# Kernel tuning notes

Hardware: AMD Instinct MI355X
Metric: run time of the kernel (lower is better)

## Reference

```python
import jax, jax.numpy as jnp
import numpy as np

V, E, HD, H, T = 50000, 256, 512, 256, 50  # vocab, embed, hidden_dim, per-direction hidden, tagset
B, S = 128, 512


def setup_inputs() -> dict:
    key = jax.random.key(0)
    ks = jax.random.split(key, 16)
    def n(k, shape, s=0.05):
        return jax.random.normal(k, shape, dtype=jnp.float32) * s
    return {
        "sentences": jax.random.randint(ks[0], (B, S), 0, V),
        "tags": jax.random.randint(ks[1], (B, S), 0, T),
        "mask": jnp.ones((B, S), dtype=bool),
        "embedding": n(ks[2], (V, E), 0.1),
        "w_ih_f": n(ks[3], (4 * H, E)), "w_hh_f": n(ks[4], (4 * H, H)),
        "b_ih_f": n(ks[5], (4 * H,)), "b_hh_f": n(ks[6], (4 * H,)),
        "w_ih_b": n(ks[7], (4 * H, E)), "w_hh_b": n(ks[8], (4 * H, H)),
        "b_ih_b": n(ks[9], (4 * H,)), "b_hh_b": n(ks[10], (4 * H,)),
        "W_out": n(ks[11], (T, HD)), "b_out": n(ks[12], (T,)),
        "start_trans": n(ks[13], (T,), 0.1),
        "end_trans": n(ks[14], (T,), 0.1),
        "trans": n(ks[15], (T, T), 0.1),
    }


def _lstm(xs, w_ih, w_hh, b, reverse):
    # xs: [S, B, E]; PyTorch gate order i, f, g, o
    Hn = w_hh.shape[1]
    def cell(carry, xt):
        h, c = carry
        g = xt @ w_ih.T + h @ w_hh.T + b
        i, f, gg, o = jnp.split(g, 4, axis=-1)
        c = jax.nn.sigmoid(f) * c + jax.nn.sigmoid(i) * jnp.tanh(gg)
        h = jax.nn.sigmoid(o) * jnp.tanh(c)
        return (h, c), h
    z = jnp.zeros((xs.shape[1], Hn), xs.dtype)
    _, hs = jax.lax.scan(cell, (z, z), xs, reverse=reverse)
    return hs  # [S, B, Hn], time-aligned with xs


def reference(sentences, tags, mask, embedding, w_ih_f, w_hh_f, b_ih_f, b_hh_f,
              w_ih_b, w_hh_b, b_ih_b, b_hh_b, W_out, b_out,
              start_trans, end_trans, trans):
    xs = jnp.swapaxes(embedding[sentences], 0, 1)           # [S, B, E]
    hf = _lstm(xs, w_ih_f, w_hh_f, b_ih_f + b_hh_f, False)
    hb = _lstm(xs, w_ih_b, w_hh_b, b_ih_b + b_hh_b, True)
    emis = jnp.concatenate([hf, hb], -1) @ W_out.T + b_out  # [S, B, T]

    tagsT = jnp.swapaxes(tags, 0, 1)                        # [S, B]
    maskT = jnp.swapaxes(mask, 0, 1)                        # [S, B] bool
    mT = maskT.astype(emis.dtype)

    # --- numerator: score of the gold path (first timestep always on, per torchcrf) ---
    emit = jnp.take_along_axis(emis, tagsT[..., None], axis=-1)[..., 0]   # [S, B]
    num = start_trans[tagsT[0]] + emit[0]
    num = num + jnp.sum((trans[tagsT[:-1], tagsT[1:]] + emit[1:]) * mT[1:], axis=0)
    last = jnp.sum(maskT.astype(jnp.int32), axis=0) - 1                    # [B]
    num = num + end_trans[tags[jnp.arange(tags.shape[0]), last]]

    # --- denominator: log-partition via forward algorithm (logsumexp scan) ---
    alpha0 = start_trans[None, :] + emis[0]                 # [B, T]
    def step(alpha, inp):
        e_t, m_t = inp
        nxt = jax.nn.logsumexp(alpha[:, :, None] + trans[None] + e_t[:, None, :], axis=1)
        return jnp.where(m_t[:, None], nxt, alpha), None
    alpha, _ = jax.lax.scan(step, alpha0, (emis[1:], maskT[1:]))
    logZ = jax.nn.logsumexp(alpha + end_trans[None, :], axis=1)

    # model returns -crf(...) with reduction='mean'
    return -jnp.mean(num - logZ)
```

## Files before the change

kernel.cpp:

```cpp
#include <hip/hip_runtime.h>

typedef __bf16 bf16x8 __attribute__((ext_vector_type(8)));
typedef float f32x4 __attribute__((ext_vector_type(4)));
typedef float f32x2 __attribute__((ext_vector_type(2)));
typedef int i32x8 __attribute__((ext_vector_type(8)));
typedef unsigned short ushort_t;
typedef unsigned int u32x4 __attribute__((ext_vector_type(4)));
typedef long i64_t;

constexpr int Ee = 256;
constexpr int HDd = 512;
constexpr int Hh = 256;
constexpr int Tt = 50;
constexpr int Bb = 128;
constexpr int Ss = 512;
constexpr int G4 = 1024;
constexpr int SB = Ss * Bb;
constexpr int Tc = 64;
constexpr int NP = Ss / Tc;
constexpr int HSTR = 272;
constexpr int NSLOT = 16;

constexpr float LOG2E = 1.4426950408889634f;
constexpr float K2f = 2.8853900817779268f;

#define DI __device__ __forceinline__

DI float bf2f(ushort_t u) {
    unsigned int x = ((unsigned int)u) << 16;
    return __builtin_bit_cast(float, x);
}
DI ushort_t f2bf(float f) {
    unsigned int x = __builtin_bit_cast(unsigned int, f);
    x += 0x7fffu + ((x >> 16) & 1u);
    return (ushort_t)(x >> 16);
}
DI bf16x8 cvt8(const float* p) {
    bf16x8 r;
#pragma unroll
    for (int i = 0; i < 8; ++i) r[i] = (__bf16)p[i];
    return r;
}
DI unsigned int pk4_fp8(float a, float b, float c, float d) {
    int v = __builtin_amdgcn_cvt_pk_fp8_f32(a, b, 0, false);
    v = __builtin_amdgcn_cvt_pk_fp8_f32(c, d, v, true);
    return (unsigned int)v;
}
DI unsigned char fp8_1(float a) {
    return (unsigned char)(__builtin_amdgcn_cvt_pk_fp8_f32(a, 0.f, 0, false) & 0xff);
}
DI float rcpf(float x) { return __builtin_amdgcn_rcpf(x); }

#if __has_builtin(__builtin_amdgcn_exp2f)
DI float ex2(float x) { return __builtin_amdgcn_exp2f(x); }
DI float ex2n(float x) { return __builtin_amdgcn_exp2f(-x); }
#else
DI float ex2(float x) {
    float r;
    asm("v_exp_f32 %0, %1\n\ts_nop 0" : "=v"(r) : "v"(x));
    return r;
}
DI float ex2n(float x) {
    float r;
    asm("v_exp_f32 %0, -%1\n\ts_nop 0" : "=v"(r) : "v"(x));
    return r;
}
#endif

DI void lds_barrier() {
    asm volatile("" ::: "memory");
    __builtin_amdgcn_s_waitcnt(0xC07F);
    __builtin_amdgcn_s_barrier();
    asm volatile("" ::: "memory");
}

__global__ void k_prep(const float* __restrict__ wihf, const float* __restrict__ whhf,
                       const float* __restrict__ wihb, const float* __restrict__ whhb,
                       const float* __restrict__ wout,
                       const float* __restrict__ bihf, const float* __restrict__ bhhf,
                       const float* __restrict__ bihb, const float* __restrict__ bhhb,
                       ushort_t* __restrict__ Wihf, ushort_t* __restrict__ Wihb,
                       unsigned char* __restrict__ Whhf8, unsigned char* __restrict__ Whhb8,
                       unsigned char* __restrict__ Wout8,
                       float* __restrict__ biasf, float* __restrict__ biasb,
                       unsigned int* __restrict__ flags) {
    int i = blockIdx.x * 256 + threadIdx.x;
    if (i < G4 * Ee) {
        float s = (((i >> 16) & 3) == 2) ? K2f : LOG2E;
        Wihf[i] = f2bf(wihf[i] * s);
        Wihb[i] = f2bf(wihb[i] * s);
    }
    if (i < G4 * Hh / 4) {
        int base = i * 4;
        float s = (((i >> 14) & 3) == 2) ? K2f : LOG2E;
        ((unsigned int*)Whhf8)[i] = pk4_fp8(whhf[base] * s, whhf[base + 1] * s,
                                            whhf[base + 2] * s, whhf[base + 3] * s);
        ((unsigned int*)Whhb8)[i] = pk4_fp8(whhb[base] * s, whhb[base + 1] * s,
                                            whhb[base + 2] * s, whhb[base + 3] * s);
    }
    if (i < 64 * HDd) Wout8[i] = 0;
    if (i < Tt * HDd) Wout8[i] = fp8_1(wout[i]);
    if (i < G4) {
        float s = (((i >> 8) & 3) == 2) ? K2f : LOG2E;
        biasf[i] = (bihf[i] + bhhf[i]) * s;
        biasb[i] = (bihb[i] + bhhb[i]) * s;
    }
    if (i < 16) flags[i] = 0;
}

struct PhaseArgs {
    const int* sentences;
    const float* emb;
    const ushort_t* Wihf;
    const ushort_t* Wihb;
    const float* biasf;
    const float* biasb;
    const unsigned char* Whhf8;
    const unsigned char* Whhb8;
    unsigned char* Gbuf;
    unsigned char* Hcat8;
    unsigned int* flags;
};

__global__ __launch_bounds__(512, 2) void k_phase(PhaseArgs a) {
    __shared__ unsigned char hring[NSLOT][16][HSTR];
    const size_t CH = (size_t)Tc * Bb * G4;
    int blk = blockIdx.x;
    int tid = threadIdx.x;

    if (blk < 16) {
        int ln = tid & 15, qd = (tid >> 4) & 3, w = tid >> 6;
        int dir = blk >> 3;
        int b0 = (blk & 7) * 16;
        const unsigned char* Whh8 = dir ? a.Whhb8 : a.Whhf8;
        int jc0 = w * 32 + ln;

        i32x8 wreg[2][4][2];
#pragma unroll
        for (int ct = 0; ct < 2; ++ct)
#pragma unroll
            for (int g = 0; g < 4; ++g) {
                const unsigned char* wb = Whh8 + (size_t)(g * Hh + jc0 + ct * 16) * Hh;
#pragma unroll
                for (int ks = 0; ks < 2; ++ks)
                    wreg[ct][g][ks] = *(const i32x8*)(wb + ks * 128 + qd * 32);
            }
        for (int i = tid; i < NSLOT * 16 * HSTR; i += 512) ((unsigned char*)hring)[i] = 0;
        __syncthreads();
        float creg[2][4] = {};
        int sctr = 0;

        for (int p = 0; p < NP; ++p) {
            if (tid == 0) {
                while (__hip_atomic_load(&a.flags[p], __ATOMIC_RELAXED,
                                         __HIP_MEMORY_SCOPE_AGENT) < 240u)
                    __builtin_amdgcn_s_sleep(1);
                __threadfence();
            }
            __syncthreads();

            const unsigned char* G = a.Gbuf + ((size_t)(dir * 2 + (p & 1))) * CH;
            int goff = ((dir ? (Tc - 1) : 0) * 32 + (b0 >> 2) + qd) * 4096 + jc0 * 16;
            const int gstep = dir ? -(32 * 4096) : (32 * 4096);

            u32x4 guA[2], guB[2];
#pragma unroll
            for (int ct = 0; ct < 2; ++ct)
                guA[ct] = *(const u32x4*)(G + goff + ct * 256);

            auto lstm_step = [&](u32x4(&gcur)[2], u32x4(&gnxt)[2], int step) {
                int rslot = (sctr + NSLOT - 1) & (NSLOT - 1), wslot = sctr & (NSLOT - 1);
                int goff2 = goff + gstep;
                if (step + 1 < Tc) {
#pragma unroll
                    for (int ct = 0; ct < 2; ++ct)
                        gnxt[ct] = *(const u32x4*)(G + goff2 + ct * 256);
                }
                i32x8 av2[2];
#pragma unroll
                for (int ks = 0; ks < 2; ++ks)
                    av2[ks] = *(const i32x8*)&hring[rslot][ln][ks * 128 + qd * 32];
                f32x4 acc[2][4];
#pragma unroll
                for (int ct = 0; ct < 2; ++ct)
#pragma unroll
                    for (int g = 0; g < 4; ++g) {
                        f32x2 lo = __builtin_amdgcn_cvt_pk_f32_fp8((int)gcur[ct][g], false);
                        f32x2 hi = __builtin_amdgcn_cvt_pk_f32_fp8((int)gcur[ct][g], true);
                        acc[ct][g][0] = lo[0];
                        acc[ct][g][1] = lo[1];
                        acc[ct][g][2] = hi[0];
                        acc[ct][g][3] = hi[1];
                    }
#pragma unroll
                for (int ks = 0; ks < 2; ++ks)
#pragma unroll
                    for (int ct = 0; ct < 2; ++ct)
#pragma unroll
                        for (int g = 0; g < 4; ++g)
                            acc[ct][g] = __builtin_amdgcn_mfma_scale_f32_16x16x128_f8f6f4(
                                av2[ks], wreg[ct][g][ks], acc[ct][g],
                                0, 0,
                                0, 127,
                                0, 127);
#pragma unroll
                for (int ct = 0; ct < 2; ++ct)
#pragma unroll
                    for (int reg = 0; reg < 4; ++reg) {
                        float ei = ex2n(acc[ct][0][reg]);
                        float ef = ex2n(acc[ct][1][reg]);
                        float eg = ex2(acc[ct][2][reg]);
                        float eo = ex2n(acc[ct][3][reg]);
                        float pf = 1.f + ef;
                        float pig = (1.f + ei) * (eg + 1.f);
                        float t2 = fmaf(eg, K2f, -K2f);
                        float cn = fmaf(creg[ct][reg], pig, t2 * pf) * rcpf(pf * pig);
                        creg[ct][reg] = cn;
                        float ec = ex2(cn);
                        float h = (ec - 1.f) * rcpf((1.f + eo) * (ec + 1.f));
                        hring[wslot][qd * 4 + reg][jc0 + ct * 16] = fp8_1(h);
                    }
                goff = goff2;
                lds_barrier();

                if ((sctr & 7) == 7) {
                    int tbase = sctr - 7;
                    int rid = tid >> 2;
                    int slotidx = rid >> 4, m = rid & 15;
                    int slot = (tbase + slotidx) & (NSLOT - 1);
                    int qp = tid & 3;
                    int t = dir ? (511 - (tbase + slotidx)) : (tbase + slotidx);
                    const unsigned char* src = &hring[slot][m][qp * 64];
                    unsigned char* dst = a.Hcat8 + ((size_t)(t * Bb + b0 + m)) * HDd + dir * Hh + qp * 64;
#pragma unroll
                    for (int i2 = 0; i2 < 4; ++i2) {
                        u32x4 v;
#pragma unroll
                        for (int k = 0; k < 4; ++k)
                            v[k] = *(const unsigned int*)(src + i2 * 16 + k * 4);
                        *(u32x4*)(dst + i2 * 16) = v;
                    }
                }
                ++sctr;
            };

            for (int step = 0; step < Tc; step += 2) {
                lstm_step(guA, guB, step);
                lstm_step(guB, guA, step + 1);
            }

            __syncthreads();
            if (tid == 0) atomicAdd(&a.flags[8 + p], 1u);
        }
    } else {
        int team = tid >> 8;
        int stid = tid & 255;
        int slot = (blk - 16) * 2 + team;
        int ln = stid & 15, qd = (stid >> 4) & 3, wv = stid >> 6;
        for (int q = 0; q < NP; ++q) {
            if (q >= 2) {
                if (tid == 0)
                    while (__hip_atomic_load(&a.flags[8 + q - 2], __ATOMIC_RELAXED,
                                             __HIP_MEMORY_SCOPE_AGENT) < 16u)
                        __builtin_amdgcn_s_sleep(64);
                __syncthreads();
            }
            for (int tile = slot; tile < 1024; tile += 480) {
                int dir = tile >> 9;
                int rem = tile & 511;
                int rt0 = rem >> 3, ct0 = rem & 7;
                const ushort_t* W = dir ? a.Wihb : a.Wihf;
                const float* bias = dir ? a.biasb : a.biasf;
                unsigned char* Gout = a.Gbuf + ((size_t)(dir * 2 + (q & 1))) * CH;
                int t0 = dir ? (NP - 1 - q) * Tc : q * Tc;
                int r0 = rt0 * 128 + (wv & 1) * 64;
                int n0 = ct0 * 128 + (wv >> 1) * 64;
                const float* aptr[4];
#pragma unroll
                for (int rt = 0; rt < 4; ++rt) {
                    int r = r0 + rt * 16 + ln;
                    int t = t0 + (r >> 7), b = r & 127;
                    aptr[rt] = a.emb + (size_t)a.sentences[b * Ss + t] * Ee;
                }
                int wrow[4];
#pragma unroll
                for (int ct = 0; ct < 4; ++ct) {
                    int c = n0 + ct * 16 + ln;
                    wrow[ct] = (c & 3) * 256 + (c >> 2);
                }
                f32x4 acc[4][4] = {};
                for (int ks = 0; ks < 8; ++ks) {
                    int k0 = ks * 32 + qd * 8;
                    bf16x8 av[4], bfr[4];
#pragma unroll
                    for (int rt = 0; rt < 4; ++rt) av[rt] = cvt8(aptr[rt] + k0);
#pragma unroll
                    for (int ct = 0; ct < 4; ++ct)
                        bfr[ct] = *(const bf16x8*)(W + (size_t)wrow[ct] * Ee + k0);
#pragma unroll
                    for (int rt = 0; rt < 4; ++rt)
#pragma unroll
                        for (int ct = 0; ct < 4; ++ct)
                            acc[rt][ct] = __builtin_amdgcn_mfma_f32_16x16x32_bf16(av[rt], bfr[ct], acc[rt][ct], 0, 0, 0);
                }
#pragma unroll
                for (int rt = 0; rt < 4; ++rt)
#pragma unroll
                    for (int ct = 0; ct < 4; ++ct) {
                        int c = n0 + ct * 16 + ln;
                        float bv = bias[wrow[ct]];
                        unsigned int pk = pk4_fp8(acc[rt][ct][0] + bv, acc[rt][ct][1] + bv,
                                                  acc[rt][ct][2] + bv, acc[rt][ct][3] + bv);
                        int rowq = ((r0 + rt * 16) >> 2) + qd;
                        *(unsigned int*)(Gout + (size_t)rowq * 4096 + (size_t)c * 4) = pk;
                    }
            }
            __syncthreads();
            if (tid == 0) {
                __threadfence();
                atomicAdd(&a.flags[q], 1u);
            }
        }
    }
}

__global__ __launch_bounds__(256, 2) void k_emis(const unsigned char* __restrict__ Hcat8,
                                                 const unsigned char* __restrict__ Wout8,
                                                 const float* __restrict__ bout,
                                                 float* __restrict__ emis) {
    int tid = threadIdx.x;
    int ln = tid & 15, qd = (tid >> 4) & 3, w = tid >> 6;
    int r0 = blockIdx.x * 128 + w * 32;
    f32x4 acc[2][4] = {};
    for (int ks = 0; ks < 16; ++ks) {
        int k0 = ks * 32 + qd * 8;
        i64_t av[2], bfr[4];
#pragma unroll
        for (int rt = 0; rt < 2; ++rt)
            av[rt] = *(const i64_t*)(Hcat8 + (size_t)(r0 + rt * 16 + ln) * HDd + k0);
#pragma unroll
        for (int ct = 0; ct < 4; ++ct)
            bfr[ct] = *(const i64_t*)(Wout8 + (size_t)(ct * 16 + ln) * HDd + k0);
#pragma unroll
        for (int rt = 0; rt < 2; ++rt)
#pragma unroll
            for (int ct = 0; ct < 4; ++ct)
                acc[rt][ct] = __builtin_amdgcn_mfma_f32_16x16x32_fp8_fp8(av[rt], bfr[ct], acc[rt][ct], 0, 0, 0);
    }
#pragma unroll
    for (int rt = 0; rt < 2; ++rt)
#pragma unroll
        for (int ct = 0; ct < 4; ++ct) {
            int j = ct * 16 + ln;
            if (j < Tt) {
                float bv = bout[j];
#pragma unroll
                for (int reg = 0; reg < 4; ++reg) {
                    int row = r0 + rt * 16 + qd * 4 + reg;
                    int t = row >> 7, b = row & 127;
                    emis[((size_t)b * Ss + t) * Tt + j] = acc[rt][ct][reg] + bv;
                }
            }
        }
}

__global__ __launch_bounds__(64) void k_crf(const float* __restrict__ emis,
                                            const float* __restrict__ start_trans,
                                            const float* __restrict__ end_trans,
                                            const float* __restrict__ trans,
                                            float* __restrict__ logZ) {
    __shared__ float E_s[64];
    int j = threadIdx.x;
    int b = blockIdx.x;
    const float* eb = emis + (size_t)b * Ss * Tt;

    float preg[52];
    preg[50] = 0.f;
    preg[51] = 0.f;
#pragma unroll
    for (int i = 0; i < Tt; ++i)
        preg[i] = (j < Tt) ? __expf(trans[i * Tt + j]) : 0.f;

    float astart = (j < Tt) ? (start_trans[j] + eb[j]) : 0.f;
    float a0 = __builtin_amdgcn_readfirstlane(astart);
    float vcur = (j < Tt) ? __expf(astart - a0) : 0.f;
    float logacc = a0;
    E_s[j] = vcur;

    float ecur[8], enxt[8];
#pragma unroll
    for (int i = 0; i < 8; ++i)
        ecur[i] = (j < Tt && 1 + i < Ss) ? eb[(1 + i) * Tt + j] : 0.f;

    for (int tb = 1; tb < Ss; tb += 8) {
#pragma unroll
        for (int i = 0; i < 8; ++i) {
            int tn = tb + 8 + i;
            enxt[i] = (j < Tt && tn < Ss) ? eb[(size_t)tn * Tt + j] : 0.f;
        }
        float ex[8];
#pragma unroll
        for (int i = 0; i < 8; ++i) ex[i] = __expf(ecur[i]);
#pragma unroll
        for (int i = 0; i < 8; ++i) {
            int t = tb + i;
            if (t >= Ss) break;
            float s0 = 0.f, s1 = 0.f, s2 = 0.f, s3 = 0.f;
#pragma unroll
            for (int i4 = 0; i4 < 13; ++i4) {
                f32x4 ev = *(const f32x4*)&E_s[i4 * 4];
                s0 = fmaf(ev[0], preg[i4 * 4 + 0], s0);
                s1 = fmaf(ev[1], preg[i4 * 4 + 1], s1);
                s2 = fmaf(ev[2], preg[i4 * 4 + 2], s2);
                s3 = fmaf(ev[3], preg[i4 * 4 + 3], s3);
            }
            vcur = ((s0 + s1) + (s2 + s3)) * ex[i];
            if (i == 3) {
                float n = __builtin_amdgcn_readfirstlane(vcur);
                vcur *= rcpf(n);
                logacc += __logf(n);
            }
            E_s[j] = vcur;
        }
        float n = __builtin_amdgcn_readfirstlane(vcur);
        vcur *= rcpf(n);
        E_s[j] = vcur;
        logacc += __logf(n);
#pragma unroll
        for (int i = 0; i < 8; ++i) ecur[i] = enxt[i];
    }
    float ve = (j < Tt) ? vcur * __expf(end_trans[j]) : 0.f;
    for (int off = 32; off > 0; off >>= 1) ve += __shfl_down(ve, off, 64);
    if (j == 0) logZ[b] = logacc + __logf(ve);
}

__global__ __launch_bounds__(256) void k_num(const int* __restrict__ tags,
                                             const float* __restrict__ emis,
                                             const float* __restrict__ trans,
                                             const float* __restrict__ start_trans,
                                             const float* __restrict__ end_trans,
                                             float* __restrict__ num) {
    __shared__ float red[4];
    int b = blockIdx.x, tid = threadIdx.x;
    const float* eb = emis + (size_t)b * Ss * Tt;
    float v = 0.f;
    for (int t = 1 + tid; t < Ss; t += 256) {
        int tp = tags[b * Ss + t - 1], tc = tags[b * Ss + t];
        v += trans[tp * Tt + tc] + eb[(size_t)t * Tt + tc];
    }
    if (tid == 0) {
        int t0 = tags[b * Ss + 0];
        v += start_trans[t0] + eb[t0] + end_trans[tags[b * Ss + Ss - 1]];
    }
    for (int off = 32; off > 0; off >>= 1) v += __shfl_down(v, off, 64);
    if ((tid & 63) == 0) red[tid >> 6] = v;
    __syncthreads();
    if (tid == 0) num[b] = red[0] + red[1] + red[2] + red[3];
}

__global__ __launch_bounds__(128) void k_out(const float* __restrict__ num,
                                             const float* __restrict__ logZ,
                                             float* __restrict__ out) {
    __shared__ float red[2];
    int b = threadIdx.x;
    float v = num[b] - logZ[b];
    for (int off = 32; off > 0; off >>= 1) v += __shfl_down(v, off, 64);
    if ((b & 63) == 0) red[b >> 6] = v;
    __syncthreads();
    if (b == 0) out[0] = -(red[0] + red[1]) / 128.f;
}

extern "C" void kernel_launch(void* const* d_in, const int* in_sizes, int n_in,
                              void* d_out, int out_size, void* d_ws, size_t ws_size,
                              hipStream_t stream) {
    const int* sentences = (const int*)d_in[0];
    const int* tags = (const int*)d_in[1];
    const float* emb = (const float*)d_in[3];
    const float* wihf = (const float*)d_in[4];
    const float* whhf = (const float*)d_in[5];
    const float* bihf = (const float*)d_in[6];
    const float* bhhf = (const float*)d_in[7];
    const float* wihb = (const float*)d_in[8];
    const float* whhb = (const float*)d_in[9];
    const float* bihb = (const float*)d_in[10];
    const float* bhhb = (const float*)d_in[11];
    const float* wout = (const float*)d_in[12];
    const float* bout = (const float*)d_in[13];
    const float* start_trans = (const float*)d_in[14];
    const float* end_trans = (const float*)d_in[15];
    const float* trans = (const float*)d_in[16];

    char* ws = (char*)d_ws;
    size_t off = 0;
    auto alloc = [&](size_t bytes) {
        void* p = ws + off;
        off += (bytes + 255) & ~(size_t)255;
        return p;
    };
    ushort_t* Wihf = (ushort_t*)alloc((size_t)G4 * Ee * 2);
    ushort_t* Wihb = (ushort_t*)alloc((size_t)G4 * Ee * 2);
    unsigned char* Whhf8 = (unsigned char*)alloc((size_t)G4 * Hh);
    unsigned char* Whhb8 = (unsigned char*)alloc((size_t)G4 * Hh);
    unsigned char* Wout8 = (unsigned char*)alloc((size_t)64 * HDd);
    float* biasf = (float*)alloc(G4 * 4);
    float* biasb = (float*)alloc(G4 * 4);
    unsigned char* Gbuf = (unsigned char*)alloc((size_t)4 * Tc * Bb * G4);
    unsigned char* Hcat8 = (unsigned char*)alloc((size_t)SB * HDd);
    float* emis = (float*)alloc((size_t)SB * Tt * 4);
    float* logZ = (float*)alloc(Bb * 4);
    float* num = (float*)alloc(Bb * 4);
    unsigned int* flags = (unsigned int*)alloc(64 * 4);
    (void)ws_size; (void)in_sizes; (void)n_in; (void)out_size;

    k_prep<<<dim3((G4 * Ee + 255) / 256), dim3(256), 0, stream>>>(
        wihf, whhf, wihb, whhb, wout, bihf, bhhf, bihb, bhhb,
        Wihf, Wihb, Whhf8, Whhb8, Wout8, biasf, biasb, flags);

    PhaseArgs pa;
    pa.sentences = sentences;
    pa.emb = emb;
    pa.Wihf = Wihf;
    pa.Wihb = Wihb;
    pa.biasf = biasf;
    pa.biasb = biasb;
    pa.Whhf8 = Whhf8;
    pa.Whhb8 = Whhb8;
    pa.Gbuf = Gbuf;
    pa.Hcat8 = Hcat8;
    pa.flags = flags;
    void* kargs[] = {&pa};
    hipLaunchCooperativeKernel((void*)k_phase, dim3(256), dim3(512), kargs, 0, stream);

    k_emis<<<dim3(SB / 128), dim3(256), 0, stream>>>(Hcat8, Wout8, bout, emis);

    k_crf<<<dim3(Bb), dim3(64), 0, stream>>>(emis, start_trans, end_trans, trans, logZ);

    k_num<<<dim3(Bb), dim3(256), 0, stream>>>(tags, emis, trans, start_trans, end_trans, num);

    k_out<<<dim3(1), dim3(128), 0, stream>>>(num, logZ, (float*)d_out);
}
```

Measured before the change: 1.301 ms.

## Fuse emission GEMM, CRF forward, numerator and final reduction into persistent cooperative kernel

Moves the emission projection, CRF log-partition scan, gold-path score and final mean into the tail of the cooperative LSTM kernel. Grid-wide atomic flag barriers replace the separate kernel launches. The intent is to remove four launch gaps and the host-side serialization between them. In exchange, the CRF scan now runs on only 64 threads of 128 large blocks, and spin barriers add synchronization cost.

```diff
diff --git a/kernel.cpp b/kernel.cpp
--- a/kernel.cpp
+++ b/kernel.cpp
@@ -105,11 +105,12 @@
         biasf[i] = (bihf[i] + bhhf[i]) * s;
         biasb[i] = (bihb[i] + bhhb[i]) * s;
     }
-    if (i < 16) flags[i] = 0;
+    if (i < 32) flags[i] = 0;
 }
 
 struct PhaseArgs {
     const int* sentences;
+    const int* tags;
     const float* emb;
     const ushort_t* Wihf;
     const ushort_t* Wihb;
@@ -117,8 +118,17 @@
     const float* biasb;
     const unsigned char* Whhf8;
     const unsigned char* Whhb8;
+    const unsigned char* Wout8;
+    const float* bout;
+    const float* start_trans;
+    const float* end_trans;
+    const float* trans;
     unsigned char* Gbuf;
     unsigned char* Hcat8;
+    float* emis;
+    float* logZ;
+    float* num;
+    float* out;
     unsigned int* flags;
 };
 
@@ -250,7 +260,10 @@
             }
 
             __syncthreads();
-            if (tid == 0) atomicAdd(&a.flags[8 + p], 1u);
+            if (tid == 0) {
+                if (p == NP - 1) __threadfence();
+                atomicAdd(&a.flags[8 + p], 1u);
+            }
         }
     } else {
         int team = tid >> 8;
@@ -322,152 +335,176 @@
             }
         }
     }
-}
-
-__global__ __launch_bounds__(256, 2) void k_emis(const unsigned char* __restrict__ Hcat8,
-                                                 const unsigned char* __restrict__ Wout8,
-                                                 const float* __restrict__ bout,
-                                                 float* __restrict__ emis) {
-    int tid = threadIdx.x;
-    int ln = tid & 15, qd = (tid >> 4) & 3, w = tid >> 6;
-    int r0 = blockIdx.x * 128 + w * 32;
-    f32x4 acc[2][4] = {};
-    for (int ks = 0; ks < 16; ++ks) {
-        int k0 = ks * 32 + qd * 8;
-        i64_t av[2], bfr[4];
+
+    if (tid == 0) {
+        while (__hip_atomic_load(&a.flags[15], __ATOMIC_RELAXED,
+                                 __HIP_MEMORY_SCOPE_AGENT) < 16u)
+            __builtin_amdgcn_s_sleep(16);
+        __threadfence();
+    }
+    __syncthreads();
+    {
+        int ln = tid & 15, qd = (tid >> 4) & 3, w = tid >> 6;
+        int r0 = blk * 256 + w * 32;
+        f32x4 acc[2][4] = {};
+        for (int ks = 0; ks < 16; ++ks) {
+            int k0 = ks * 32 + qd * 8;
+            i64_t av[2], bfr[4];
+#pragma unroll
+            for (int rt = 0; rt < 2; ++rt)
+                av[rt] = *(const i64_t*)(a.Hcat8 + (size_t)(r0 + rt * 16 + ln) * HDd + k0);
+#pragma unroll
+            for (int ct = 0; ct < 4; ++ct)
+                bfr[ct] = *(const i64_t*)(a.Wout8 + (size_t)(ct * 16 + ln) * HDd + k0);
+#pragma unroll
+            for (int rt = 0; rt < 2; ++rt)
+#pragma unroll
+                for (int ct = 0; ct < 4; ++ct)
+                    acc[rt][ct] = __builtin_amdgcn_mfma_f32_16x16x32_fp8_fp8(av[rt], bfr[ct], acc[rt][ct], 0, 0, 0);
+        }
 #pragma unroll
         for (int rt = 0; rt < 2; ++rt)
-            av[rt] = *(const i64_t*)(Hcat8 + (size_t)(r0 + rt * 16 + ln) * HDd + k0);
-#pragma unroll
-        for (int ct = 0; ct < 4; ++ct)
-            bfr[ct] = *(const i64_t*)(Wout8 + (size_t)(ct * 16 + ln) * HDd + k0);
-#pragma unroll
-        for (int rt = 0; rt < 2; ++rt)
-#pragma unroll
-            for (int ct = 0; ct < 4; ++ct)
-                acc[rt][ct] = __builtin_amdgcn_mfma_f32_16x16x32_fp8_fp8(av[rt], bfr[ct], acc[rt][ct], 0, 0, 0);
-    }
-#pragma unroll
-    for (int rt = 0; rt < 2; ++rt)
-#pragma unroll
-        for (int ct = 0; ct < 4; ++ct) {
-            int j = ct * 16 + ln;
-            if (j < Tt) {
-                float bv = bout[j];
-#pragma unroll
-                for (int reg = 0; reg < 4; ++reg) {
-                    int row = r0 + rt * 16 + qd * 4 + reg;
-                    int t = row >> 7, b = row & 127;
-                    emis[((size_t)b * Ss + t) * Tt + j] = acc[rt][ct][reg] + bv;
-                }
-            }
-        }
-}
-
-__global__ __launch_bounds__(64) void k_crf(const float* __restrict__ emis,
-                                            const float* __restrict__ start_trans,
-                                            const float* __restrict__ end_trans,
-                                            const float* __restrict__ trans,
-                                            float* __restrict__ logZ) {
-    __shared__ float E_s[64];
-    int j = threadIdx.x;
-    int b = blockIdx.x;
-    const float* eb = emis + (size_t)b * Ss * Tt;
-
-    float preg[52];
-    preg[50] = 0.f;
-    preg[51] = 0.f;
-#pragma unroll
-    for (int i = 0; i < Tt; ++i)
-        preg[i] = (j < Tt) ? __expf(trans[i * Tt + j]) : 0.f;
-
-    float astart = (j < Tt) ? (start_trans[j] + eb[j]) : 0.f;
-    float a0 = __builtin_amdgcn_readfirstlane(astart);
-    float vcur = (j < Tt) ? __expf(astart - a0) : 0.f;
-    float logacc = a0;
-    E_s[j] = vcur;
-
-    float ecur[8], enxt[8];
-#pragma unroll
-    for (int i = 0; i < 8; ++i)
-        ecur[i] = (j < Tt && 1 + i < Ss) ? eb[(1 + i) * Tt + j] : 0.f;
-
-    for (int tb = 1; tb < Ss; tb += 8) {
-#pragma unroll
-        for (int i = 0; i < 8; ++i) {
-            int tn = tb + 8 + i;
-            enxt[i] = (j < Tt && tn < Ss) ? eb[(size_t)tn * Tt + j] : 0.f;
-        }
-        float ex[8];
-#pragma unroll
-        for (int i = 0; i < 8; ++i) ex[i] = __expf(ecur[i]);
-#pragma unroll
-        for (int i = 0; i < 8; ++i) {
-            int t = tb + i;
-            if (t >= Ss) break;
-            float s0 = 0.f, s1 = 0.f, s2 = 0.f, s3 = 0.f;
-#pragma unroll
-            for (int i4 = 0; i4 < 13; ++i4) {
-                f32x4 ev = *(const f32x4*)&E_s[i4 * 4];
-                s0 = fmaf(ev[0], preg[i4 * 4 + 0], s0);
-                s1 = fmaf(ev[1], preg[i4 * 4 + 1], s1);
-                s2 = fmaf(ev[2], preg[i4 * 4 + 2], s2);
-                s3 = fmaf(ev[3], preg[i4 * 4 + 3], s3);
-            }
-            vcur = ((s0 + s1) + (s2 + s3)) * ex[i];
-            if (i == 3) {
+#pragma unroll
+            for (int ct = 0; ct < 4; ++ct) {
+                int j = ct * 16 + ln;
+                if (j < Tt) {
+                    float bv = a.bout[j];
+#pragma unroll
+                    for (int reg = 0; reg < 4; ++reg) {
+                        int row = r0 + rt * 16 + qd * 4 + reg;
+                        int t = row >> 7, b = row & 127;
+                        a.emis[((size_t)b * Ss + t) * Tt + j] = acc[rt][ct][reg] + bv;
+                    }
+                }
+            }
+    }
+    __syncthreads();
+    if (tid == 0) {
+        __threadfence();
+        atomicAdd(&a.flags[16], 1u);
+        while (__hip_atomic_load(&a.flags[16], __ATOMIC_RELAXED,
+                                 __HIP_MEMORY_SCOPE_AGENT) < 256u)
+            __builtin_amdgcn_s_sleep(16);
+        __threadfence();
+    }
+    __syncthreads();
+
+    if (blk < 128) {
+        if (tid < 64) {
+            float* E_s = (float*)&hring[0][0][0];
+            int j = tid;
+            int b = blk;
+            const float* eb = a.emis + (size_t)b * Ss * Tt;
+
+            float preg[52];
+            preg[50] = 0.f;
+            preg[51] = 0.f;
+#pragma unroll
+            for (int i = 0; i < Tt; ++i)
+                preg[i] = (j < Tt) ? __expf(a.trans[i * Tt + j]) : 0.f;
+
+            float astart = (j < Tt) ? (a.start_trans[j] + eb[j]) : 0.f;
+            float a0 = __builtin_amdgcn_readfirstlane(astart);
+            float vcur = (j < Tt) ? __expf(astart - a0) : 0.f;
+            float logacc = a0;
+            E_s[j] = vcur;
+
+            float ecur[8], enxt[8];
+#pragma unroll
+            for (int i = 0; i < 8; ++i)
+                ecur[i] = (j < Tt && 1 + i < Ss) ? eb[(1 + i) * Tt + j] : 0.f;
+
+            for (int tb = 1; tb < Ss; tb += 8) {
+#pragma unroll
+                for (int i = 0; i < 8; ++i) {
+                    int tn = tb + 8 + i;
+                    enxt[i] = (j < Tt && tn < Ss) ? eb[(size_t)tn * Tt + j] : 0.f;
+                }
+                float ex[8];
+#pragma unroll
+                for (int i = 0; i < 8; ++i) ex[i] = __expf(ecur[i]);
+#pragma unroll
+                for (int i = 0; i < 8; ++i) {
+                    int t = tb + i;
+                    if (t >= Ss) break;
+                    float s0 = 0.f, s1 = 0.f, s2 = 0.f, s3 = 0.f;
+#pragma unroll
+                    for (int i4 = 0; i4 < 13; ++i4) {
+                        f32x4 ev = *(const f32x4*)&E_s[i4 * 4];
+                        s0 = fmaf(ev[0], preg[i4 * 4 + 0], s0);
+                        s1 = fmaf(ev[1], preg[i4 * 4 + 1], s1);
+                        s2 = fmaf(ev[2], preg[i4 * 4 + 2], s2);
+                        s3 = fmaf(ev[3], preg[i4 * 4 + 3], s3);
+                    }
+                    vcur = ((s0 + s1) + (s2 + s3)) * ex[i];
+                    if (i == 3) {
+                        float n = __builtin_amdgcn_readfirstlane(vcur);
+                        vcur *= rcpf(n);
+                        logacc += __logf(n);
+                    }
+                    E_s[j] = vcur;
+                }
                 float n = __builtin_amdgcn_readfirstlane(vcur);
                 vcur *= rcpf(n);
+                E_s[j] = vcur;
                 logacc += __logf(n);
-            }
-            E_s[j] = vcur;
-        }
-        float n = __builtin_amdgcn_readfirstlane(vcur);
-        vcur *= rcpf(n);
-        E_s[j] = vcur;
-        logacc += __logf(n);
-#pragma unroll
-        for (int i = 0; i < 8; ++i) ecur[i] = enxt[i];
-    }
-    float ve = (j < Tt) ? vcur * __expf(end_trans[j]) : 0.f;
-    for (int off = 32; off > 0; off >>= 1) ve += __shfl_down(ve, off, 64);
-    if (j == 0) logZ[b] = logacc + __logf(ve);
-}
-
-__global__ __launch_bounds__(256) void k_num(const int* __restrict__ tags,
-                                             const float* __restrict__ emis,
-                                             const float* __restrict__ trans,
-                                             const float* __restrict__ start_trans,
-                                             const float* __restrict__ end_trans,
-                                             float* __restrict__ num) {
-    __shared__ float red[4];
-    int b = blockIdx.x, tid = threadIdx.x;
-    const float* eb = emis + (size_t)b * Ss * Tt;
-    float v = 0.f;
-    for (int t = 1 + tid; t < Ss; t += 256) {
-        int tp = tags[b * Ss + t - 1], tc = tags[b * Ss + t];
-        v += trans[tp * Tt + tc] + eb[(size_t)t * Tt + tc];
-    }
+#pragma unroll
+                for (int i = 0; i < 8; ++i) ecur[i] = enxt[i];
+            }
+            float ve = (j < Tt) ? vcur * __expf(a.end_trans[j]) : 0.f;
+            for (int off = 32; off > 0; off >>= 1) ve += __shfl_down(ve, off, 64);
+            if (j == 0) a.logZ[b] = logacc + __logf(ve);
+        }
+    } else {
+        float* red = (float*)&hring[1][0][0];
+        int b = blk - 128;
+        const float* eb = a.emis + (size_t)b * Ss * Tt;
+        float v = 0.f;
+        int t = 1 + tid;
+        if (t < Ss) {
+            int tp = a.tags[b * Ss + t - 1], tc = a.tags[b * Ss + t];
+            v = a.trans[tp * Tt + tc] + eb[(size_t)t * Tt + tc];
+        }
+        if (tid == 0) {
+            int t0 = a.tags[b * Ss + 0];
+            v += a.start_trans[t0] + eb[t0] + a.end_trans[a.tags[b * Ss + Ss - 1]];
+        }
+        for (int off = 32; off > 0; off >>= 1) v += __shfl_down(v, off, 64);
+        if ((tid & 63) == 0) red[tid >> 6] = v;
+        __syncthreads();
+        if (tid == 0) {
+            float s = 0.f;
+#pragma unroll
+            for (int i = 0; i < 8; ++i) s += red[i];
+            a.num[b] = s;
+        }
+    }
+    __syncthreads();
     if (tid == 0) {
-        int t0 = tags[b * Ss + 0];
-        v += start_trans[t0] + eb[t0] + end_trans[tags[b * Ss + Ss - 1]];
-    }
-    for (int off = 32; off > 0; off >>= 1) v += __shfl_down(v, off, 64);
-    if ((tid & 63) == 0) red[tid >> 6] = v;
-    __syncthreads();
-    if (tid == 0) num[b] = red[0] + red[1] + red[2] + red[3];
-}
-
-__global__ __launch_bounds__(128) void k_out(const float* __restrict__ num,
-                                             const float* __restrict__ logZ,
-                                             float* __restrict__ out) {
-    __shared__ float red[2];
-    int b = threadIdx.x;
-    float v = num[b] - logZ[b];
-    for (int off = 32; off > 0; off >>= 1) v += __shfl_down(v, off, 64);
-    if ((b & 63) == 0) red[b >> 6] = v;
-    __syncthreads();
-    if (b == 0) out[0] = -(red[0] + red[1]) / 128.f;
+        __threadfence();
+        atomicAdd(&a.flags[17], 1u);
+    }
+
+    if (blk == 0) {
+        if (tid == 0) {
+            while (__hip_atomic_load(&a.flags[17], __ATOMIC_RELAXED,
+                                     __HIP_MEMORY_SCOPE_AGENT) < 256u)
+                __builtin_amdgcn_s_sleep(16);
+            __threadfence();
+        }
+        __syncthreads();
+        float* red = (float*)&hring[2][0][0];
+        float v = (tid < 128) ? (a.num[tid] - a.logZ[tid]) : 0.f;
+        for (int off = 32; off > 0; off >>= 1) v += __shfl_down(v, off, 64);
+        if ((tid & 63) == 0) red[tid >> 6] = v;
+        __syncthreads();
+        if (tid == 0) {
+            float s = 0.f;
+#pragma unroll
+            for (int i = 0; i < 8; ++i) s += red[i];
+            a.out[0] = -s / 128.f;
+        }
+    }
 }
 
 extern "C" void kernel_launch(void* const* d_in, const int* in_sizes, int n_in,
@@ -518,6 +555,7 @@
 
     PhaseArgs pa;
     pa.sentences = sentences;
+    pa.tags = tags;
     pa.emb = emb;
     pa.Wihf = Wihf;
     pa.Wihb = Wihb;
@@ -525,17 +563,18 @@
     pa.biasb = biasb;
     pa.Whhf8 = Whhf8;
     pa.Whhb8 = Whhb8;
+    pa.Wout8 = Wout8;
+    pa.bout = bout;
+    pa.start_trans = start_trans;
+    pa.end_trans = end_trans;
+    pa.trans = trans;
     pa.Gbuf = Gbuf;
     pa.Hcat8 = Hcat8;
+    pa.emis = emis;
+    pa.logZ = logZ;
+    pa.num = num;
+    pa.out = (float*)d_out;
     pa.flags = flags;
     void* kargs[] = {&pa};
     hipLaunchCooperativeKernel((void*)k_phase, dim3(256), dim3(512), kargs, 0, stream);
-
-    k_emis<<<dim3(SB / 128), dim3(256), 0, stream>>>(Hcat8, Wout8, bout, emis);
-
-    k_crf<<<dim3(Bb), dim3(64), 0, stream>>>(emis, start_trans, end_trans, trans, logZ);
-
-    k_num<<<dim3(Bb), dim3(256), 0, stream>>>(tags, emis, trans, start_trans, end_trans, num);
-
-    k_out<<<dim3(1), dim3(128), 0, stream>>>(num, logZ, (float*)d_out);
-}
+}
```

Result: no change. 1.295 ms (-0.5%).
